# Kernel optimization log

Measured on AMD Instinct MI355X. Metric: run time of the kernel, lower is better.

Reference implementation:

```python
import jax, jax.numpy as jnp
import numpy as np


def setup_inputs() -> dict:
    key = jax.random.key(0)
    k1, k2 = jax.random.split(key)
    B, L, D = 8, 2048, 128
    x1 = jax.random.normal(k1, (B, L, D), dtype=jnp.float32)
    x2 = jax.random.normal(k2, (B, L, D), dtype=jnp.float32)
    return {"x1": x1, "x2": x2}


def reference(x1, x2):
    # attention[b, i, j] = <x1[b,i,:], x2[b,j,:]>   -> [B, L1, L2]
    attention = jnp.einsum("bid,bjd->bij", x1, x2)
    # softmax over axis=1 (rows / L1) and axis=2 (cols / L2)
    w_att_1 = jax.nn.softmax(attention, axis=1)              # [B, L1, L2]
    w_att_2 = jnp.swapaxes(jax.nn.softmax(attention, axis=2), 1, 2)  # [B, L2, L1]
    # Dot(axes=1): contract the sequence axis 1
    in1_aligned = jnp.einsum("bij,bid->bjd", w_att_1, x1)    # [B, L2, D]
    in2_aligned = jnp.einsum("bji,bjd->bid", w_att_2, x2)    # [B, L1, D]
    # submult(a, b) = concat([a - b, a * b]); combined = concat([a, b, a-b, a*b])
    q1_combined = jnp.concatenate(
        [x1, in2_aligned, x1 - in2_aligned, x1 * in2_aligned], axis=-1)  # [B, L1, 4D]
    q2_combined = jnp.concatenate(
        [x2, in1_aligned, x2 - in1_aligned, x2 * in1_aligned], axis=-1)  # [B, L2, 4D]
    return q1_combined, q2_combined
```

## Files before the change

kernel.cpp:

```cpp
#include <hip/hip_runtime.h>


typedef __bf16    bf16;
typedef _Float16  f16;
typedef __bf16    bf16x4 __attribute__((ext_vector_type(4)));
typedef _Float16  f16x4  __attribute__((ext_vector_type(4)));
typedef __bf16    bf16x8 __attribute__((ext_vector_type(8)));
typedef _Float16  f16x8  __attribute__((ext_vector_type(8)));
typedef float     floatx4 __attribute__((ext_vector_type(4)));
typedef unsigned int uintx4 __attribute__((ext_vector_type(4)));

#define NB 8
#define SL 2048
#define TI 64
#define NT 32

#define F16SZ (NB * SL * 128 * 2)

#define SKV_S  136
#define SVT_S  32

#define OFF_VT   8704
#define GSPAN    16896
#define OFF_L    33792
#define LDS_BYTES 34048

__global__ __launch_bounds__(256)
void prepass_cvt(const float* __restrict__ x1, const float* __restrict__ x2,
                 char* __restrict__ ws)
{
    __shared__ float tile[64 * 129];
    const int tid = threadIdx.x;
    const int j0  = blockIdx.x * 64;
    const int b   = blockIdx.y;
    const int z   = blockIdx.z;
    const float* src = z ? x2 : x1;
    f16*  oF = (f16*) (ws + (size_t)z * F16SZ);
    bf16* oT = (bf16*)(ws + 2 * (size_t)F16SZ + (size_t)z * F16SZ);

    #pragma unroll
    for (int n = 0; n < 8; ++n) {
        int ci = n * 256 + tid;
        int row = ci >> 5, c4 = ci & 31;
        const float4 v = *(const float4*)(src + ((size_t)b * SL + j0 + row) * 128 + c4 * 4);
        tile[row * 129 + c4 * 4 + 0] = v.x;
        tile[row * 129 + c4 * 4 + 1] = v.y;
        tile[row * 129 + c4 * 4 + 2] = v.z;
        tile[row * 129 + c4 * 4 + 3] = v.w;
        f16x4 h; h[0] = (f16)v.x; h[1] = (f16)v.y; h[2] = (f16)v.z; h[3] = (f16)v.w;
        *(f16x4*)(oF + ((size_t)b * SL + j0 + row) * 128 + c4 * 4) = h;
    }
    __syncthreads();
    #pragma unroll
    for (int n = 0; n < 8; ++n) {
        int fi = n * 256 + tid;
        int jg = fi & 15, d = fi >> 4;
        bf16x4 o;
        #pragma unroll
        for (int i = 0; i < 4; ++i) o[i] = (bf16)tile[(jg * 4 + i) * 129 + d];
        *(bf16x4*)(oT + ((size_t)b * 128 + d) * SL + j0 + jg * 4) = o;
    }
}

__global__ __launch_bounds__(256, 2)
void soft_attn_align_mfma(const float* __restrict__ x1,
                          const float* __restrict__ x2,
                          const char* __restrict__ ws,
                          float* __restrict__ out)
{
    __shared__ __align__(16) char lds_raw[LDS_BYTES];

    const int tid  = threadIdx.x;
    const int lane = tid & 63;
    const int wv   = tid >> 6;
    const int g    = wv >> 1;
    const int rowbase = (wv & 1) * 32;
    const int lr   = lane & 15;
    const int lq   = lane >> 4;
    const int t128 = tid & 127;

    char* gb   = lds_raw + g * GSPAN;
    f16*   sKV  = (f16*) (gb);
    bf16*  sVT  = (bf16*)(gb + OFF_VT);
    float* aOut = (float*)(lds_raw);
    float* sL   = (float*)(lds_raw + OFF_L);

    const int i0  = blockIdx.x * TI;
    const int bi  = blockIdx.y;
    const int dir = blockIdx.z;

    const float* xq = dir ? x2 : x1;
    const f16*  x1f = (const f16*)(ws);
    const f16*  x2f = (const f16*)(ws + F16SZ);
    const bf16* x1T = (const bf16*)(ws + 2 * (size_t)F16SZ);
    const bf16* x2T = (const bf16*)(ws + 3 * (size_t)F16SZ);
    const f16*  xqf  = dir ? x2f : x1f;
    const f16*  xkvf = dir ? x1f : x2f;
    const bf16* xvT  = dir ? x1T : x2T;

    f16x8 aQ[2][4];
    #pragma unroll
    for (int rb = 0; rb < 2; ++rb) {
        const f16* qrow = xqf + ((size_t)bi * SL + i0 + rowbase + rb * 16 + lr) * 128;
        #pragma unroll
        for (int kk = 0; kk < 4; ++kk)
            aQ[rb][kk] = *(const f16x8*)(qrow + kk * 32 + lq * 8);
    }

    float   l_acc[2] = {0.f, 0.f};
    floatx4 Oacc[2][8];
    #pragma unroll
    for (int rb = 0; rb < 2; ++rb)
        #pragma unroll
        for (int nd = 0; nd < 8; ++nd) Oacc[rb][nd] = (floatx4){0.f, 0.f, 0.f, 0.f};

    const int rowK = t128 >> 4, colK = t128 & 15;
    const int dV0  = t128 >> 2, jcV  = t128 & 3;
    const f16*  kvf = xkvf + ((size_t)bi * SL + g * 1024 + rowK) * 128 + colK * 8;
    const bf16* vTf = xvT + ((size_t)bi * 128 + dV0) * SL + g * 1024 + jcV * 8;

    f16x8  kreg[4];
    bf16x8 vreg[4];
    {
        #pragma unroll
        for (int n = 0; n < 4; ++n) {
            kreg[n] = *(const f16x8*)(kvf + (size_t)n * 8 * 128);
            vreg[n] = *(const bf16x8*)(vTf + (size_t)n * 32 * SL);
        }
    }

    for (int t = 0; t < NT; ++t) {
        __syncthreads();

        #pragma unroll
        for (int n = 0; n < 4; ++n) {
            *(f16x8*) (sKV + (rowK + n * 8) * SKV_S + colK * 8) = kreg[n];
            *(bf16x8*)(sVT + (dV0 + n * 32) * SVT_S + jcV * 8)  = vreg[n];
        }
        __syncthreads();

        if (t < NT - 1) {
            const f16*  kb = kvf + (size_t)(t + 1) * 32 * 128;
            const bf16* vb = vTf + (size_t)(t + 1) * 32;
            #pragma unroll
            for (int n = 0; n < 4; ++n) {
                kreg[n] = *(const f16x8*)(kb + (size_t)n * 8 * 128);
                vreg[n] = *(const bf16x8*)(vb + (size_t)n * 32 * SL);
            }
        }

        floatx4 Sf[2][2];
        Sf[0][0] = (floatx4){0.f,0.f,0.f,0.f}; Sf[0][1] = (floatx4){0.f,0.f,0.f,0.f};
        Sf[1][0] = (floatx4){0.f,0.f,0.f,0.f}; Sf[1][1] = (floatx4){0.f,0.f,0.f,0.f};
        __builtin_amdgcn_s_setprio(1);
        #pragma unroll
        for (int kk = 0; kk < 4; ++kk) {
            f16x8 aK0 = *(const f16x8*)(sKV + (lr)      * SKV_S + kk * 32 + lq * 8);
            f16x8 aK1 = *(const f16x8*)(sKV + (16 + lr) * SKV_S + kk * 32 + lq * 8);
            Sf[0][0] = __builtin_amdgcn_mfma_f32_16x16x32_f16(aK0, aQ[0][kk], Sf[0][0], 0, 0, 0);
            Sf[0][1] = __builtin_amdgcn_mfma_f32_16x16x32_f16(aK1, aQ[0][kk], Sf[0][1], 0, 0, 0);
            Sf[1][0] = __builtin_amdgcn_mfma_f32_16x16x32_f16(aK0, aQ[1][kk], Sf[1][0], 0, 0, 0);
            Sf[1][1] = __builtin_amdgcn_mfma_f32_16x16x32_f16(aK1, aQ[1][kk], Sf[1][1], 0, 0, 0);
        }
        __builtin_amdgcn_s_setprio(0);

        bf16x8 aP[2];
        #pragma unroll
        for (int rb = 0; rb < 2; ++rb) {
            float p00 = __expf(Sf[rb][0][0]), p01 = __expf(Sf[rb][0][1]);
            float p02 = __expf(Sf[rb][0][2]), p03 = __expf(Sf[rb][0][3]);
            float p10 = __expf(Sf[rb][1][0]), p11 = __expf(Sf[rb][1][1]);
            float p12 = __expf(Sf[rb][1][2]), p13 = __expf(Sf[rb][1][3]);
            l_acc[rb] += ((p00 + p01) + (p02 + p03)) + ((p10 + p11) + (p12 + p13));

            unsigned int A0, B0, A1, B1;
            asm("v_cvt_pk_bf16_f32 %0, %1, %2" : "=v"(A0) : "v"(p00), "v"(p01));
            asm("v_cvt_pk_bf16_f32 %0, %1, %2" : "=v"(B0) : "v"(p02), "v"(p03));
            asm("v_cvt_pk_bf16_f32 %0, %1, %2" : "=v"(A1) : "v"(p10), "v"(p11));
            asm("v_cvt_pk_bf16_f32 %0, %1, %2" : "=v"(B1) : "v"(p12), "v"(p13));
            asm("v_permlane32_swap_b32 %0, %1" : "+v"(A0), "+v"(A1));
            asm("v_permlane16_swap_b32 %0, %1" : "+v"(A0), "+v"(A1));
            asm("v_permlane32_swap_b32 %0, %1" : "+v"(B0), "+v"(B1));
            asm("v_permlane16_swap_b32 %0, %1" : "+v"(B0), "+v"(B1));
            uintx4 fr; fr.x = A0; fr.y = B0; fr.z = A1; fr.w = B1;
            aP[rb] = __builtin_bit_cast(bf16x8, fr);
        }

        __builtin_amdgcn_s_setprio(1);
        #pragma unroll
        for (int nd = 0; nd < 8; ++nd) {
            bf16x8 bV = *(const bf16x8*)(sVT + (nd * 16 + lr) * SVT_S + lq * 8);
            Oacc[0][nd] = __builtin_amdgcn_mfma_f32_16x16x32_bf16(aP[0], bV, Oacc[0][nd], 0, 0, 0);
            Oacc[1][nd] = __builtin_amdgcn_mfma_f32_16x16x32_bf16(aP[1], bV, Oacc[1][nd], 0, 0, 0);
        }
        __builtin_amdgcn_s_setprio(0);
    }

    float l_row[2][4];
    #pragma unroll
    for (int rb = 0; rb < 2; ++rb) {
        float lv = l_acc[rb];
        lv += __shfl_xor(lv, 16, 64);
        lv += __shfl_xor(lv, 32, 64);
        #pragma unroll
        for (int r = 0; r < 4; ++r)
            l_row[rb][r] = __shfl(lv, lq * 4 + r, 64);
    }

    __syncthreads();

    if (g == 1) {
        #pragma unroll
        for (int rb = 0; rb < 2; ++rb)
            #pragma unroll
            for (int r = 0; r < 4; ++r) {
                int row = rowbase + rb * 16 + lq * 4 + r;
                #pragma unroll
                for (int nd = 0; nd < 8; ++nd)
                    aOut[row * 132 + nd * 16 + lr] = Oacc[rb][nd][r];
                if (lr == 0) sL[row] = l_row[rb][r];
            }
    }
    __syncthreads();
    if (g == 0) {
        #pragma unroll
        for (int rb = 0; rb < 2; ++rb)
            #pragma unroll
            for (int r = 0; r < 4; ++r) {
                int row = rowbase + rb * 16 + lq * 4 + r;
                float inv = 1.0f / (l_row[rb][r] + sL[row]);
                #pragma unroll
                for (int nd = 0; nd < 8; ++nd) {
                    int idx = row * 132 + nd * 16 + lr;
                    aOut[idx] = (Oacc[rb][nd][r] + aOut[idx]) * inv;
                }
            }
    }
    __syncthreads();

    float* outb = out + ((size_t)dir * NB * SL + (size_t)bi * SL + i0) * 512;
    #pragma unroll
    for (int k = 0; k < 8; ++k) {
        int s = tid + 256 * k;
        int r = s >> 5, c4 = s & 31;
        float4 a = *(const float4*)(aOut + r * 132 + c4 * 4);
        float4 q = *(const float4*)(xq + ((size_t)bi * SL + i0 + r) * 128 + c4 * 4);
        float4 d, m;
        d.x = q.x - a.x; d.y = q.y - a.y; d.z = q.z - a.z; d.w = q.w - a.w;
        m.x = q.x * a.x; m.y = q.y * a.y; m.z = q.z * a.z; m.w = q.w * a.w;
        float4* orow = (float4*)(outb + (size_t)r * 512);
        orow[c4]      = q;
        orow[32 + c4] = a;
        orow[64 + c4] = d;
        orow[96 + c4] = m;
    }
}

extern "C" void kernel_launch(void* const* d_in, const int* in_sizes, int n_in,
                              void* d_out, int out_size, void* d_ws, size_t ws_size,
                              hipStream_t stream) {
    const float* x1 = (const float*)d_in[0];
    const float* x2 = (const float*)d_in[1];
    float* out = (float*)d_out;
    (void)in_sizes; (void)n_in; (void)out_size; (void)ws_size;

    dim3 pgrid(SL / 64, NB, 2);
    prepass_cvt<<<pgrid, dim3(256), 0, stream>>>(x1, x2, (char*)d_ws);

    dim3 grid(SL / TI, NB, 2);
    soft_attn_align_mfma<<<grid, dim3(256), 0, stream>>>(x1, x2, (const char*)d_ws, out);
}
```

Baseline: 130.6 us.

## Double key/value tile width to 64 per iteration and defer V prefetch

Each group now processes 64 keys per loop iteration instead of 32, halving the number of iterations and barriers while doubling the LDS staging buffers and register prefetch buffers. The V-tile prefetch is moved after the exponent/softmax stage so its global loads overlap the P·V MFMAs rather than competing with the score computation. The larger LDS footprint (about 70KB) and doubled prefetch registers may reduce occupancy from the requested 2 blocks per CU.

```diff
diff --git a/kernel.cpp b/kernel.cpp
--- a/kernel.cpp
+++ b/kernel.cpp
@@ -13,17 +13,18 @@
 #define NB 8
 #define SL 2048
 #define TI 64
-#define NT 32
+#define TJ 64
+#define NT 16
 
 #define F16SZ (NB * SL * 128 * 2)
 
 #define SKV_S  136
-#define SVT_S  32
-
-#define OFF_VT   8704
-#define GSPAN    16896
-#define OFF_L    33792
-#define LDS_BYTES 34048
+#define SVT_S  68
+
+#define OFF_VT   17408
+#define GSPAN    34816
+#define OFF_L    69632
+#define LDS_BYTES 69888
 
 __global__ __launch_bounds__(256)
 void prepass_cvt(const float* __restrict__ x1, const float* __restrict__ x2,
@@ -79,9 +80,9 @@
     const int lq   = lane >> 4;
     const int t128 = tid & 127;
 
-    char* gb   = lds_raw + g * GSPAN;
-    f16*   sKV  = (f16*) (gb);
-    bf16*  sVT  = (bf16*)(gb + OFF_VT);
+    char* gb  = lds_raw + g * GSPAN;
+    f16*  sKV = (f16*) (gb);
+    bf16* sVT = (bf16*)(gb + OFF_VT);
     float* aOut = (float*)(lds_raw);
     float* sL   = (float*)(lds_raw + OFF_L);
 
@@ -107,7 +108,7 @@
             aQ[rb][kk] = *(const f16x8*)(qrow + kk * 32 + lq * 8);
     }
 
-    float   l_acc[2] = {0.f, 0.f};
+    float l_acc[2] = {0.f, 0.f};
     floatx4 Oacc[2][8];
     #pragma unroll
     for (int rb = 0; rb < 2; ++rb)
@@ -119,79 +120,94 @@
     const f16*  kvf = xkvf + ((size_t)bi * SL + g * 1024 + rowK) * 128 + colK * 8;
     const bf16* vTf = xvT + ((size_t)bi * 128 + dV0) * SL + g * 1024 + jcV * 8;
 
-    f16x8  kreg[4];
-    bf16x8 vreg[4];
+    f16x8  kreg[8];
+    bf16x8 vreg[8];
     {
         #pragma unroll
-        for (int n = 0; n < 4; ++n) {
+        for (int n = 0; n < 8; ++n)
             kreg[n] = *(const f16x8*)(kvf + (size_t)n * 8 * 128);
-            vreg[n] = *(const bf16x8*)(vTf + (size_t)n * 32 * SL);
-        }
+        #pragma unroll
+        for (int n = 0; n < 8; ++n)
+            vreg[n] = *(const bf16x8*)(vTf + (size_t)(n & 3) * 32 * SL + (n >> 2) * 32);
     }
 
     for (int t = 0; t < NT; ++t) {
         __syncthreads();
 
         #pragma unroll
-        for (int n = 0; n < 4; ++n) {
-            *(f16x8*) (sKV + (rowK + n * 8) * SKV_S + colK * 8) = kreg[n];
-            *(bf16x8*)(sVT + (dV0 + n * 32) * SVT_S + jcV * 8)  = vreg[n];
-        }
+        for (int n = 0; n < 8; ++n)
+            *(f16x8*)(sKV + (rowK + n * 8) * SKV_S + colK * 8) = kreg[n];
+        #pragma unroll
+        for (int n = 0; n < 8; ++n)
+            *(bf16x8*)(sVT + (dV0 + (n & 3) * 32) * SVT_S + (jcV + 4 * (n >> 2)) * 8) = vreg[n];
         __syncthreads();
 
         if (t < NT - 1) {
-            const f16*  kb = kvf + (size_t)(t + 1) * 32 * 128;
-            const bf16* vb = vTf + (size_t)(t + 1) * 32;
-            #pragma unroll
-            for (int n = 0; n < 4; ++n) {
+            const f16* kb = kvf + (size_t)(t + 1) * TJ * 128;
+            #pragma unroll
+            for (int n = 0; n < 8; ++n)
                 kreg[n] = *(const f16x8*)(kb + (size_t)n * 8 * 128);
-                vreg[n] = *(const bf16x8*)(vb + (size_t)n * 32 * SL);
-            }
-        }
-
-        floatx4 Sf[2][2];
-        Sf[0][0] = (floatx4){0.f,0.f,0.f,0.f}; Sf[0][1] = (floatx4){0.f,0.f,0.f,0.f};
-        Sf[1][0] = (floatx4){0.f,0.f,0.f,0.f}; Sf[1][1] = (floatx4){0.f,0.f,0.f,0.f};
+        }
+
+        floatx4 Sf[2][4];
+        #pragma unroll
+        for (int rb = 0; rb < 2; ++rb)
+            #pragma unroll
+            for (int jj = 0; jj < 4; ++jj)
+                Sf[rb][jj] = (floatx4){0.f, 0.f, 0.f, 0.f};
         __builtin_amdgcn_s_setprio(1);
         #pragma unroll
         for (int kk = 0; kk < 4; ++kk) {
-            f16x8 aK0 = *(const f16x8*)(sKV + (lr)      * SKV_S + kk * 32 + lq * 8);
-            f16x8 aK1 = *(const f16x8*)(sKV + (16 + lr) * SKV_S + kk * 32 + lq * 8);
-            Sf[0][0] = __builtin_amdgcn_mfma_f32_16x16x32_f16(aK0, aQ[0][kk], Sf[0][0], 0, 0, 0);
-            Sf[0][1] = __builtin_amdgcn_mfma_f32_16x16x32_f16(aK1, aQ[0][kk], Sf[0][1], 0, 0, 0);
-            Sf[1][0] = __builtin_amdgcn_mfma_f32_16x16x32_f16(aK0, aQ[1][kk], Sf[1][0], 0, 0, 0);
-            Sf[1][1] = __builtin_amdgcn_mfma_f32_16x16x32_f16(aK1, aQ[1][kk], Sf[1][1], 0, 0, 0);
+            #pragma unroll
+            for (int jj = 0; jj < 4; ++jj) {
+                f16x8 aK = *(const f16x8*)(sKV + (jj * 16 + lr) * SKV_S + kk * 32 + lq * 8);
+                Sf[0][jj] = __builtin_amdgcn_mfma_f32_16x16x32_f16(aK, aQ[0][kk], Sf[0][jj], 0, 0, 0);
+                Sf[1][jj] = __builtin_amdgcn_mfma_f32_16x16x32_f16(aK, aQ[1][kk], Sf[1][jj], 0, 0, 0);
+            }
         }
         __builtin_amdgcn_s_setprio(0);
 
-        bf16x8 aP[2];
+        bf16x8 aP[2][2];
         #pragma unroll
         for (int rb = 0; rb < 2; ++rb) {
-            float p00 = __expf(Sf[rb][0][0]), p01 = __expf(Sf[rb][0][1]);
-            float p02 = __expf(Sf[rb][0][2]), p03 = __expf(Sf[rb][0][3]);
-            float p10 = __expf(Sf[rb][1][0]), p11 = __expf(Sf[rb][1][1]);
-            float p12 = __expf(Sf[rb][1][2]), p13 = __expf(Sf[rb][1][3]);
-            l_acc[rb] += ((p00 + p01) + (p02 + p03)) + ((p10 + p11) + (p12 + p13));
-
-            unsigned int A0, B0, A1, B1;
-            asm("v_cvt_pk_bf16_f32 %0, %1, %2" : "=v"(A0) : "v"(p00), "v"(p01));
-            asm("v_cvt_pk_bf16_f32 %0, %1, %2" : "=v"(B0) : "v"(p02), "v"(p03));
-            asm("v_cvt_pk_bf16_f32 %0, %1, %2" : "=v"(A1) : "v"(p10), "v"(p11));
-            asm("v_cvt_pk_bf16_f32 %0, %1, %2" : "=v"(B1) : "v"(p12), "v"(p13));
-            asm("v_permlane32_swap_b32 %0, %1" : "+v"(A0), "+v"(A1));
-            asm("v_permlane16_swap_b32 %0, %1" : "+v"(A0), "+v"(A1));
-            asm("v_permlane32_swap_b32 %0, %1" : "+v"(B0), "+v"(B1));
-            asm("v_permlane16_swap_b32 %0, %1" : "+v"(B0), "+v"(B1));
-            uintx4 fr; fr.x = A0; fr.y = B0; fr.z = A1; fr.w = B1;
-            aP[rb] = __builtin_bit_cast(bf16x8, fr);
+            #pragma unroll
+            for (int ks = 0; ks < 2; ++ks) {
+                float p00 = __expf(Sf[rb][2 * ks][0]), p01 = __expf(Sf[rb][2 * ks][1]);
+                float p02 = __expf(Sf[rb][2 * ks][2]), p03 = __expf(Sf[rb][2 * ks][3]);
+                float p10 = __expf(Sf[rb][2 * ks + 1][0]), p11 = __expf(Sf[rb][2 * ks + 1][1]);
+                float p12 = __expf(Sf[rb][2 * ks + 1][2]), p13 = __expf(Sf[rb][2 * ks + 1][3]);
+                l_acc[rb] += ((p00 + p01) + (p02 + p03)) + ((p10 + p11) + (p12 + p13));
+
+                unsigned int A0, B0, A1, B1;
+                asm("v_cvt_pk_bf16_f32 %0, %1, %2" : "=v"(A0) : "v"(p00), "v"(p01));
+                asm("v_cvt_pk_bf16_f32 %0, %1, %2" : "=v"(B0) : "v"(p02), "v"(p03));
+                asm("v_cvt_pk_bf16_f32 %0, %1, %2" : "=v"(A1) : "v"(p10), "v"(p11));
+                asm("v_cvt_pk_bf16_f32 %0, %1, %2" : "=v"(B1) : "v"(p12), "v"(p13));
+                asm("v_permlane32_swap_b32 %0, %1" : "+v"(A0), "+v"(A1));
+                asm("v_permlane16_swap_b32 %0, %1" : "+v"(A0), "+v"(A1));
+                asm("v_permlane32_swap_b32 %0, %1" : "+v"(B0), "+v"(B1));
+                asm("v_permlane16_swap_b32 %0, %1" : "+v"(B0), "+v"(B1));
+                uintx4 fr; fr.x = A0; fr.y = B0; fr.z = A1; fr.w = B1;
+                aP[rb][ks] = __builtin_bit_cast(bf16x8, fr);
+            }
+        }
+
+        if (t < NT - 1) {
+            const bf16* vb = vTf + (size_t)(t + 1) * TJ;
+            #pragma unroll
+            for (int n = 0; n < 8; ++n)
+                vreg[n] = *(const bf16x8*)(vb + (size_t)(n & 3) * 32 * SL + (n >> 2) * 32);
         }
 
         __builtin_amdgcn_s_setprio(1);
         #pragma unroll
         for (int nd = 0; nd < 8; ++nd) {
-            bf16x8 bV = *(const bf16x8*)(sVT + (nd * 16 + lr) * SVT_S + lq * 8);
-            Oacc[0][nd] = __builtin_amdgcn_mfma_f32_16x16x32_bf16(aP[0], bV, Oacc[0][nd], 0, 0, 0);
-            Oacc[1][nd] = __builtin_amdgcn_mfma_f32_16x16x32_bf16(aP[1], bV, Oacc[1][nd], 0, 0, 0);
+            bf16x8 bV0 = *(const bf16x8*)(sVT + (nd * 16 + lr) * SVT_S + lq * 8);
+            bf16x8 bV1 = *(const bf16x8*)(sVT + (nd * 16 + lr) * SVT_S + 32 + lq * 8);
+            Oacc[0][nd] = __builtin_amdgcn_mfma_f32_16x16x32_bf16(aP[0][0], bV0, Oacc[0][nd], 0, 0, 0);
+            Oacc[0][nd] = __builtin_amdgcn_mfma_f32_16x16x32_bf16(aP[0][1], bV1, Oacc[0][nd], 0, 0, 0);
+            Oacc[1][nd] = __builtin_amdgcn_mfma_f32_16x16x32_bf16(aP[1][0], bV0, Oacc[1][nd], 0, 0, 0);
+            Oacc[1][nd] = __builtin_amdgcn_mfma_f32_16x16x32_bf16(aP[1][1], bV1, Oacc[1][nd], 0, 0, 0);
         }
         __builtin_amdgcn_s_setprio(0);
     }
```

New measurement: 191.4 us. +46.5%, slower.
